# Kernel optimization log

Hardware: AMD Instinct MI355X
Metric: run time of the kernel (lower is better)

Reference implementation:

```python
import jax, jax.numpy as jnp
import numpy as np

B, N, L, D = 4096, 11, 12, 256
ZDIM = 32
LINE_DIM = 64
PAST_DIM = 6 * D - (2 * D + LINE_DIM)  # 960


def _pos_enc(length, d):
    # PositionalAgentEncoding.build_pos_enc
    pos = jnp.arange(length, dtype=jnp.float32)[:, None]
    div = jnp.exp(jnp.arange(0, d, 2, dtype=jnp.float32) * (-np.log(10000.0) / d))
    pe = jnp.zeros((length, d), dtype=jnp.float32)
    pe = pe.at[:, 0::2].set(jnp.sin(pos * div))
    pe = pe.at[:, 1::2].set(jnp.cos(pos * div))
    return pe


def setup_inputs() -> dict:
    key = jax.random.key(0)
    ks = jax.random.split(key, 16)
    s = 0.02
    return {
        "inputs": jax.random.normal(ks[0], (B * N, L, 4), jnp.float32),
        "past_feature": jax.random.normal(ks[1], (B * N, PAST_DIM), jnp.float32),
        "W_in": jax.random.normal(ks[2], (4, D), jnp.float32) * s,
        "b_in": jnp.zeros((D,), jnp.float32),
        "W_pos": jax.random.normal(ks[3], (2 * D, D), jnp.float32) * s,
        "b_pos": jnp.zeros((D,), jnp.float32),
        "W_fc2": jax.random.normal(ks[4], (L * D, D), jnp.float32) * s,
        "b_fc2": jnp.zeros((D,), jnp.float32),
        "W_fc3": jax.random.normal(ks[5], (D + N, D), jnp.float32) * s,
        "b_fc3": jnp.zeros((D,), jnp.float32),
        "W_msg": jax.random.normal(ks[6], (2 * D, D), jnp.float32) * s,
        "b_msg": jnp.zeros((D,), jnp.float32),
        "W_hyp": jax.random.normal(ks[7], (2 * D, D), jnp.float32) * s,
        "b_hyp": jnp.zeros((D,), jnp.float32),
        "W_line": jax.random.normal(ks[8], (D, LINE_DIM), jnp.float32) * s,
        "W_out": jax.random.normal(ks[9], (6 * D, 128), jnp.float32) * s,
        "b_out": jnp.zeros((128,), jnp.float32),
        "W_qz": jax.random.normal(ks[10], (128, 2 * ZDIM), jnp.float32) * s,
        "b_qz": jnp.zeros((2 * ZDIM,), jnp.float32),
        "batch_size": B,
        "agent_num": N,
    }


def reference(inputs, past_feature, W_in, b_in, W_pos, b_pos, W_fc2, b_fc2,
              W_fc3, b_fc3, W_msg, b_msg, W_hyp, b_hyp, W_line,
              W_out, b_out, W_qz, b_qz, batch_size, agent_num):
    BN, length, _ = inputs.shape
    d = W_in.shape[1]
    bsz, n = batch_size, agent_num
    # input_fc + positional encoding (concat=True, dropout=eval identity)
    tf = inputs @ W_in + b_in                                   # [BN, L, D]
    pe = jnp.broadcast_to(_pos_enc(length, d), (BN, length, d))
    tf = jnp.concatenate([tf, pe], axis=-1) @ W_pos + b_pos     # [BN, L, D]
    # input_fc2 over flattened time, then category concat + input_fc3
    ftraj = tf.reshape(bsz, n, length * d) @ W_fc2 + b_fc2      # [B, N, D]
    cat = jnp.broadcast_to(jnp.eye(n, dtype=ftraj.dtype), (bsz, n, n))
    ftraj = jnp.concatenate([ftraj, cat], axis=-1) @ W_fc3 + b_fc3
    # cosine correlation + per-scene adaptive threshold
    q = ftraj / jnp.linalg.norm(ftraj, axis=2, keepdims=True)
    corr = jnp.einsum('bnd,bmd->bnm', q, q)                     # [B, N, N]
    a = corr.min(axis=(1, 2))
    thr = jnp.where(a < 0.4, 0.4,
                    jnp.where((a > 0.4) & (a < 0.6), a + 0.1, a + 0.03))
    corr = jnp.where(corr < thr[:, None, None], 0.0, corr)
    # ordinary MS_HGNN surrogate: one dense message-passing round
    attn = jax.nn.softmax(jnp.einsum('bnd,bmd->bnm', ftraj, ftraj)
                          / jnp.sqrt(jnp.asarray(d, ftraj.dtype)), axis=-1)
    agg = jnp.einsum('bnm,bmd->bnd', attn, ftraj)
    ftraj_inter = jax.nn.relu(jnp.concatenate([ftraj, agg], -1) @ W_msg + b_msg)
    # hyper/clique surrogate: binarized thresholded corr as incidence, degree-normalized
    A = (corr > 0).astype(ftraj.dtype)
    A = A / jnp.maximum(A.sum(-1, keepdims=True), 1.0)
    hag = jnp.einsum('bnm,bmd->bnd', A, ftraj)
    hyp = jax.nn.relu(jnp.concatenate([ftraj, hag], -1) @ W_hyp + b_hyp)
    feat_bs = hyp @ W_line                                      # [B, N, 64]
    final = jnp.concatenate([ftraj, ftraj_inter, feat_bs], -1).reshape(bsz * n, -1)
    h = jnp.concatenate([past_feature, final], axis=-1)         # [BN, 6D]
    h = jax.nn.relu(h @ W_out + b_out)
    return h @ W_qz + b_qz                                      # [BN, 2*zdim]
```

## Files before the change

### kernel.cpp

```cpp
#include <hip/hip_runtime.h>
#include <hip/hip_bf16.h>

#define BB 4096
#define NNA 11
#define BN (BB*NNA)

#define OFF_WEFF   0
#define OFF_BIASL  1024
#define OFF_WBIG   4096
#define OFF_BIAS2  16384
#define OFF_WALL   16640
#define OFF_BIASN  28928
#define OFF_WG1F   31744
#define OFF_BIASG1 87040
#define OFF_WG2    99712
#define OFF_WQT    198656
#define OFF_P2T    202752
#define OFF_P3T    205824
#define OFF_MIX    296320
#define OFF_INTER  1287552

typedef short bh8 __attribute__((ext_vector_type(8)));
typedef float fx4 __attribute__((ext_vector_type(4)));

__device__ __forceinline__ short f2bs(float v) { __hip_bfloat16 h = __float2bfloat16(v); return *(short*)&h; }

typedef __attribute__((address_space(1))) const void __gptr_t;
typedef __attribute__((address_space(3))) void __lptr_t;
__device__ __forceinline__ void gload_lds16(const void* g, void* l) {
  __builtin_amdgcn_global_load_lds((__gptr_t*)g, (__lptr_t*)l, 16, 0, 0);
}


__global__ __launch_bounds__(256) void k_p1(const float* W_in, const float* b_in,
                                            const float* W_pos, const float* b_pos,
                                            float* ws) {
  __shared__ float A[16*512];
  __shared__ float red[4*16*64];
  int t = threadIdx.x, cb = blockIdx.x;
  int ks = t >> 6, c = t & 63, col = cb*64 + c;
  float coef = -logf(10000.f) / 256.f;
  for (int i = t; i < 16*512; i += 256) {
    int row = i >> 9, kk = i & 511;
    float v;
    if (row < 4) v = (kk < 256) ? W_in[row*256 + kk] : 0.f;
    else if (kk < 256) v = b_in[kk];
    else {
      int ii = (kk - 256) >> 1;
      float dv = expf(coef * (float)(2*ii));
      float ang = (float)(row - 4) * dv;
      v = (kk & 1) ? cosf(ang) : sinf(ang);
    }
    A[i] = v;
  }
  __syncthreads();
  float acc[16];
  #pragma unroll
  for (int r = 0; r < 16; ++r) acc[r] = 0.f;
  #pragma unroll 4
  for (int j = 0; j < 128; ++j) {
    int jj = ks*128 + j;
    float b = W_pos[(size_t)jj*256 + col];
    #pragma unroll
    for (int r = 0; r < 16; ++r) acc[r] += A[r*512 + jj] * b;
  }
  #pragma unroll
  for (int r = 0; r < 16; ++r) red[(ks*16 + r)*64 + c] = acc[r];
  __syncthreads();
  for (int i = t; i < 16*64; i += 256) {
    int row = i >> 6, cc = i & 63;
    float s = red[row*64+cc] + red[(16+row)*64+cc] + red[(32+row)*64+cc] + red[(48+row)*64+cc];
    int gcol = cb*64 + cc;
    if (row < 4) ws[OFF_WEFF + row*256 + gcol] = s;
    else         ws[OFF_BIASL + (row-4)*256 + gcol] = s + b_pos[gcol];
  }
}

__global__ __launch_bounds__(256) void k_p2(const float* W_fc2, float* ws) {
  __shared__ float A[5*256];
  __shared__ float red[4*5*64];
  int t = threadIdx.x, cb = blockIdx.x, l = blockIdx.y;
  int ks = t >> 6, c = t & 63, col = cb*64 + c;
  for (int i = t; i < 5*256; i += 256) {
    int row = i >> 8, kk = i & 255;
    A[i] = (row < 4) ? ws[OFF_WEFF + row*256 + kk] : ws[OFF_BIASL + l*256 + kk];
  }
  __syncthreads();
  float acc[5] = {0.f, 0.f, 0.f, 0.f, 0.f};
  #pragma unroll 4
  for (int j = 0; j < 64; ++j) {
    int jj = ks*64 + j;
    float b = W_fc2[(size_t)(l*256 + jj)*256 + col];
    #pragma unroll
    for (int r = 0; r < 5; ++r) acc[r] += A[r*256 + jj] * b;
  }
  #pragma unroll
  for (int r = 0; r < 5; ++r) red[(ks*5 + r)*64 + c] = acc[r];
  __syncthreads();
  for (int i = t; i < 5*64; i += 256) {
    int row = i / 64, cc = i % 64;
    float s = red[row*64+cc] + red[(5+row)*64+cc] + red[(10+row)*64+cc] + red[(15+row)*64+cc];
    int gcol = cb*64 + cc;
    if (row < 4) ws[OFF_WBIG + (l*4 + row)*256 + gcol] = s;
    else         ws[OFF_P2T + l*256 + gcol] = s;
  }
}

__global__ __launch_bounds__(256) void k_p3(const float* W_fc3, const float* b_fc2, float* ws) {
  __shared__ float A[7*256];
  __shared__ float red[4*7*64];
  int t = threadIdx.x, cb = blockIdx.x, rg = blockIdx.y;
  int ks = t >> 6, c = t & 63, col = cb*64 + c;
  for (int i = t; i < 7*256; i += 256) {
    int row = i >> 8, kk = i & 255, gr = rg*7 + row;
    float v;
    if (gr < 48) v = ws[OFF_WBIG + gr*256 + kk];
    else {
      v = b_fc2[kk];
      #pragma unroll
      for (int l = 0; l < 12; ++l) v += ws[OFF_P2T + l*256 + kk];
    }
    A[i] = v;
  }
  __syncthreads();
  float acc[7] = {0.f,0.f,0.f,0.f,0.f,0.f,0.f};
  #pragma unroll 4
  for (int j = 0; j < 64; ++j) {
    int jj = ks*64 + j;
    float b = W_fc3[(size_t)jj*256 + col];
    #pragma unroll
    for (int r = 0; r < 7; ++r) acc[r] += A[r*256 + jj] * b;
  }
  #pragma unroll
  for (int r = 0; r < 7; ++r) red[(ks*7 + r)*64 + c] = acc[r];
  __syncthreads();
  for (int i = t; i < 7*64; i += 256) {
    int row = i / 64, cc = i % 64, gr = rg*7 + row;
    float s = red[row*64+cc] + red[(7+row)*64+cc] + red[(14+row)*64+cc] + red[(21+row)*64+cc];
    int gcol = cb*64 + cc;
    if (gr < 48)       ws[OFF_WALL + gr*256 + gcol] = s;
    else if (gr == 48) ws[OFF_P3T + gcol] = s;
  }
}

__device__ __forceinline__ float wg1_elem(int j, int col, const float* W_msg,
                                          const float* W_hyp, const float* W_out) {
  if (col < 256)       return W_msg[j*256 + col];
  else if (col < 512)  return W_msg[(256+j)*256 + (col-256)];
  else if (col < 768)  return W_hyp[j*256 + (col-512)];
  else if (col < 1024) return W_hyp[(256+j)*256 + (col-768)];
  else                 return W_out[(960+j)*128 + (col-1024)];
}

__global__ __launch_bounds__(256) void k_p4(const float* W_msg, const float* b_msg,
                                            const float* W_hyp, const float* b_hyp,
                                            const float* W_out, const float* W_fc3,
                                            const float* b_fc3, float* ws) {
  __shared__ float A[8*256];
  __shared__ float red[4*8*64];
  int t = threadIdx.x, cb = blockIdx.x, rg = blockIdx.y;
  int ks = t >> 6, c = t & 63, col = cb*64 + c;
  for (int i = t; i < 8*256; i += 256) {
    int row = i >> 8, kk = i & 255, gr = rg*8 + row;
    float v;
    if (gr < 48)      v = ws[OFF_WALL + gr*256 + kk];
    else if (gr < 59) v = ws[OFF_P3T + kk] + b_fc3[kk] + W_fc3[(size_t)(256 + gr - 48)*256 + kk];
    else              v = 0.f;
    A[i] = v;
  }
  __syncthreads();
  float acc[8];
  #pragma unroll
  for (int r = 0; r < 8; ++r) acc[r] = 0.f;
  #pragma unroll 4
  for (int j = 0; j < 64; ++j) {
    int jj = ks*64 + j;
    float b = wg1_elem(jj, col, W_msg, W_hyp, W_out);
    #pragma unroll
    for (int r = 0; r < 8; ++r) acc[r] += A[r*256 + jj] * b;
  }
  #pragma unroll
  for (int r = 0; r < 8; ++r) red[(ks*8 + r)*64 + c] = acc[r];
  __syncthreads();
  for (int i = t; i < 8*64; i += 256) {
    int row = i >> 6, cc = i & 63, gr = rg*8 + row;
    float s = red[row*64+cc] + red[(8+row)*64+cc] + red[(16+row)*64+cc] + red[(24+row)*64+cc];
    int gcol = cb*64 + cc;
    if (gr < 48) {
      ws[OFF_WG1F + gr*1152 + gcol] = s;
    } else if (gr < 59) {
      if (gcol < 256) s += b_msg[gcol];
      else if (gcol >= 512 && gcol < 768) s += b_hyp[gcol-512];
      ws[OFF_BIASG1 + (gr-48)*1152 + gcol] = s;
    }
  }
}

__global__ __launch_bounds__(128) void k_p5(const float* W_line, const float* W_out,
                                            const float* W_qz, float* ws) {
  int t = threadIdx.x;
  if (blockIdx.x >= 1536) {
    int i = (blockIdx.x - 1536)*128 + t;
    int n = i >> 7, k = i & 127;
    short* WQs = (short*)(ws + OFF_WQT);
    WQs[n*128 + k] = f2bs(W_qz[k*64 + n]);
    return;
  }
  int c = t, r = blockIdx.x;
  float v;
  if (r < 960)       v = W_out[r*128 + c];
  else if (r < 1216) v = W_out[(r+256)*128 + c];
  else if (r < 1472) {
    int dd = r - 1216;
    float s = 0.f;
    for (int j = 0; j < 64; ++j)
      s += W_line[dd*64 + j] * W_out[(1472+j)*128 + c];
    v = s;
  } else if (r < 1520) {
    v = ws[OFF_WG1F + (r-1472)*1152 + 1024 + c];
  } else v = 0.f;
  short* WTs = (short*)(ws + OFF_WG2);
  WTs[(size_t)c*1536 + r] = f2bs(v);
}

__global__ __launch_bounds__(256) void k_front(const float* inputs, const float* W_fc3,
                                               const float* b_fc3, float* ws) {
  __shared__ float XT[48*44];
  __shared__ float F[44*260];
  __shared__ float C[4*121];
  int t = threadIdx.x;
  int R0 = blockIdx.x * 44;
  for (int i = t; i < 44*48; i += 256) {
    int r = i / 48, k = i - r*48;
    XT[k*44 + r] = inputs[(size_t)(R0+r)*48 + k];
  }
  __syncthreads();
  {
    int d = t;
    float acc[44];
    float base = ws[OFF_P3T + d] + b_fc3[d];
    #pragma unroll
    for (int r = 0; r < 44; ++r) acc[r] = base + W_fc3[(size_t)(256 + (r % 11))*256 + d];
    for (int k = 0; k < 48; ++k) {
      float w = ws[OFF_WALL + k*256 + d];
      #pragma unroll
      for (int j = 0; j < 11; ++j) {
        float4 xv = *(const float4*)&XT[k*44 + 4*j];
        acc[4*j+0] += xv.x*w; acc[4*j+1] += xv.y*w;
        acc[4*j+2] += xv.z*w; acc[4*j+3] += xv.w*w;
      }
    }
    #pragma unroll
    for (int r = 0; r < 44; ++r) F[r*260 + d] = acc[r];
  }
  __syncthreads();
  int w = t >> 6, lane = t & 63;
  {
    const float4* F4 = (const float4*)F;
    for (int p = lane; p < 66; p += 64) {
      int n = 0, pp = p;
      while (pp >= 11 - n) { pp -= 11 - n; ++n; }
      int m = n + pp;
      int ra = (w*11 + n) * 65, rb2 = (w*11 + m) * 65;
      float s = 0.f;
      #pragma unroll 4
      for (int j = 0; j < 64; ++j) {
        float4 a = F4[ra + j], b = F4[rb2 + j];
        s += a.x*b.x + a.y*b.y + a.z*b.z + a.w*b.w;
      }
      C[w*121 + n*11 + m] = s;
      C[w*121 + m*11 + n] = s;
    }
  }
  __syncthreads();
  {
    float* Cw = C + w*121;
    float rn[11];
    #pragma unroll
    for (int n = 0; n < 11; ++n) rn[n] = 1.f / sqrtf(Cw[n*11+n]);
    float a = 1e30f;
    for (int n = 0; n < 11; ++n)
      for (int m = 0; m < 11; ++m)
        a = fminf(a, Cw[n*11+m] * rn[n] * rn[m]);
    float thr = (a < 0.4f) ? 0.4f : (((a > 0.4f) && (a < 0.6f)) ? a + 0.1f : a + 0.03f);
    int scene = blockIdx.x*4 + w;
    float* mixb = ws + OFF_MIX + (size_t)scene*242;
    if (lane < 11) {
      int n = lane;
      float mx = -1e30f;
      #pragma unroll
      for (int m = 0; m < 11; ++m) mx = fmaxf(mx, Cw[n*11+m]);
      mx *= (1.f/16.f);
      float e[11], ssum = 0.f;
      #pragma unroll
      for (int m = 0; m < 11; ++m) { e[m] = expf(Cw[n*11+m]*(1.f/16.f) - mx); ssum += e[m]; }
      float inv = 1.f / ssum;
      #pragma unroll
      for (int m = 0; m < 11; ++m) mixb[n*11+m] = e[m]*inv;
      float keep[11], cnt = 0.f;
      #pragma unroll
      for (int m = 0; m < 11; ++m) {
        float q = Cw[n*11+m] * rn[n] * rn[m];
        keep[m] = (q >= thr) ? 1.f : 0.f; cnt += keep[m];
      }
      float sc = 1.f / fmaxf(cnt, 1.f);
      #pragma unroll
      for (int m = 0; m < 11; ++m) mixb[121 + n*11 + m] = keep[m]*sc;
    }
  }
}

__global__ __launch_bounds__(256) void k_mix(const float* inputs, float* ws,
                                             __hip_bfloat16* outI, __hip_bfloat16* outH) {
  __shared__ float XT[48*24];
  __shared__ float MW[2*121];
  int t = threadIdx.x;
  int s0 = blockIdx.x * 2;
  int R0 = s0 * 11;
  int gy = blockIdx.y;
  __hip_bfloat16* dst = gy ? outH : outI;
  for (int i = t; i < 22*48; i += 256) {
    int r = i / 48, k = i - r*48;
    XT[k*24 + r] = inputs[(size_t)(R0+r)*48 + k];
  }
  for (int i = t; i < 96; i += 256) { int k = i >> 1, r = 22 + (i & 1); XT[k*24+r] = 0.f; }
  for (int i = t; i < 242; i += 256) {
    int s = i / 121, j = i - s*121;
    MW[i] = ws[OFF_MIX + (size_t)(s0+s)*242 + gy*121 + j];
  }
  __syncthreads();
  int gc = gy*512 + t;
  float accT[24], accB[24];
  #pragma unroll
  for (int r = 0; r < 24; ++r) {
    if (r < 22) {
      accT[r] = ws[OFF_BIASG1 + (r % 11)*1152 + gc];
      accB[r] = ws[OFF_BIASG1 + (r % 11)*1152 + gc + 256];
    } else { accT[r] = 0.f; accB[r] = 0.f; }
  }
  for (int k = 0; k < 48; ++k) {
    float wt = ws[OFF_WG1F + k*1152 + gc];
    float wb = ws[OFF_WG1F + k*1152 + gc + 256];
    #pragma unroll
    for (int j = 0; j < 6; ++j) {
      float4 xv = *(const float4*)&XT[k*24 + 4*j];
      accT[4*j+0] += xv.x*wt; accT[4*j+1] += xv.y*wt; accT[4*j+2] += xv.z*wt; accT[4*j+3] += xv.w*wt;
      accB[4*j+0] += xv.x*wb; accB[4*j+1] += xv.y*wb; accB[4*j+2] += xv.z*wb; accB[4*j+3] += xv.w*wb;
    }
  }
  #pragma unroll
  for (int s = 0; s < 2; ++s)
    #pragma unroll
    for (int n = 0; n < 11; ++n) {
      float v = accT[s*11+n];
      #pragma unroll
      for (int m = 0; m < 11; ++m)
        v += MW[s*121 + n*11 + m] * accB[s*11+m];
      v = fmaxf(v, 0.f);
      dst[(size_t)(R0 + s*11 + n)*256 + t] = __float2bfloat16(v);
    }
}

#define A_BYTE(b) ((b)*8192)
#define B_BYTE(b) (16384 + (b)*16384)
#define HS_OFF 0
#define WQ_OFF 8704
__device__ __forceinline__ int swz(int row, int kshort) {
  return row*128 + ((kshort*2) ^ ((row & 7) << 4));
}
__global__ __launch_bounds__(256) void k_g2(const float* past, const float* inputs,
                                            const float* b_out, const float* b_qz,
                                            const __hip_bfloat16* interI, const __hip_bfloat16* hypI,
                                            float* ws, float* out) {
  __shared__ short LDS[24576];
  int t = threadIdx.x;
  int R0 = blockIdx.x * 64;
  int w = t >> 6, lane = t & 63, quad = lane >> 4, l16 = lane & 15;
  const short* WTs = (const short*)(ws + OFF_WG2);
  const short* WQs = (const short*)(ws + OFF_WQT);
  const short* intS = (const short*)interI;
  const short* hypS = (const short*)hypI;
  char* LB = (char*)LDS;

  int ar = t >> 2, akq = (t & 3) * 16;
  int brr = lane >> 3, bb0 = (lane & 7) * 16;

  fx4 acc[4][2];
  #pragma unroll
  for (int mt = 0; mt < 4; ++mt)
    #pragma unroll
    for (int reg = 0; reg < 4; ++reg) {
      int nidx = (R0 + mt*16 + quad*4 + reg) % 11;
      #pragma unroll
      for (int nt = 0; nt < 2; ++nt) {
        int col = w*32 + nt*16 + l16;
        acc[mt][nt][reg] = b_out[col] + ws[OFF_BIASG1 + nidx*1152 + 1024 + col];
      }
    }

  float4 pa[4];
  bh8 pah[2];

  auto prefA = [&](int cch) {
    if (cch < 15) {
      const float4* sp = (const float4*)(past + (size_t)(R0+ar)*960 + cch*64 + akq);
      pa[0]=sp[0]; pa[1]=sp[1]; pa[2]=sp[2]; pa[3]=sp[3];
    } else if (cch < 23) {
      const short* s = ((cch < 19) ? intS : hypS) + (size_t)(R0+ar)*256 + ((cch < 19)?(cch-15):(cch-19))*64 + akq;
      pah[0] = *(const bh8*)&s[0];
      pah[1] = *(const bh8*)&s[8];
    } else {
      if (akq < 48) {
        const float4* sp = (const float4*)(inputs + (size_t)(R0+ar)*48 + akq);
        pa[0]=sp[0]; pa[1]=sp[1]; pa[2]=sp[2]; pa[3]=sp[3];
      }
    }
  };
  auto writeA = [&](int cch, int abuf) {
    if (cch < 15 || cch == 23) {
      short tmp[16];
      if (cch == 23 && akq >= 48) {
        #pragma unroll
        for (int q = 0; q < 16; ++q) tmp[q] = 0;
      } else {
        #pragma unroll
        for (int q = 0; q < 4; ++q) {
          tmp[4*q+0]=f2bs(pa[q].x); tmp[4*q+1]=f2bs(pa[q].y);
          tmp[4*q+2]=f2bs(pa[q].z); tmp[4*q+3]=f2bs(pa[q].w);
        }
      }
      *(bh8*)(LB + A_BYTE(abuf) + swz(ar, akq))     = *(bh8*)&tmp[0];
      *(bh8*)(LB + A_BYTE(abuf) + swz(ar, akq + 8)) = *(bh8*)&tmp[8];
    } else {
      *(bh8*)(LB + A_BYTE(abuf) + swz(ar, akq))     = pah[0];
      *(bh8*)(LB + A_BYTE(abuf) + swz(ar, akq + 8)) = pah[1];
    }
  };
  auto stageB = [&](int cch, int bbuf) {
    #pragma unroll
    for (int c = 0; c < 4; ++c) {
      int r = (c*4 + w)*8 + brr;
      const char* g = (const char*)(WTs + (size_t)r*1536 + cch*64) + (bb0 ^ ((r & 7) << 4));
      gload_lds16(g, LB + B_BYTE(bbuf) + (c*4 + w)*1024);
    }
  };

  prefA(0);
  stageB(0, 0);
  writeA(0, 0);
  prefA(1);
  int buf = 0;
  for (int ch = 0; ch < 24; ++ch) {
    __syncthreads();
    if (ch + 1 < 24) {
      stageB(ch + 1, buf ^ 1);
      writeA(ch + 1, buf ^ 1);
      if (ch + 2 < 24) prefA(ch + 2);
    }
    #pragma unroll
    for (int ks = 0; ks < 2; ++ks) {
      int kk = ks*32 + quad*8;
      bh8 a[4], b[2];
      #pragma unroll
      for (int mt = 0; mt < 4; ++mt)
        a[mt] = *(const bh8*)(LB + A_BYTE(buf) + swz(mt*16 + l16, kk));
      #pragma unroll
      for (int nt = 0; nt < 2; ++nt) {
        int r = w*32 + nt*16 + l16;
        b[nt] = *(const bh8*)(LB + B_BYTE(buf) + swz(r, kk));
      }
      #pragma unroll
      for (int mt = 0; mt < 4; ++mt)
        #pragma unroll
        for (int nt = 0; nt < 2; ++nt)
          acc[mt][nt] = __builtin_amdgcn_mfma_f32_16x16x32_bf16(a[mt], b[nt], acc[mt][nt], 0, 0, 0);
    }
    buf ^= 1;
  }
  __syncthreads();
  #pragma unroll
  for (int mt = 0; mt < 4; ++mt)
    #pragma unroll
    for (int nt = 0; nt < 2; ++nt)
      #pragma unroll
      for (int reg = 0; reg < 4; ++reg)
        LDS[HS_OFF + (mt*16 + quad*4 + reg)*136 + w*32 + nt*16 + l16] = f2bs(fmaxf(acc[mt][nt][reg], 0.f));
  {
    int n = t >> 2, kh = (t & 3) * 32;
    const short* s = WQs + n*128 + kh;
    #pragma unroll
    for (int q = 0; q < 4; ++q)
      *(bh8*)&LDS[WQ_OFF + n*136 + kh + q*8] = *(const bh8*)&s[q*8];
  }
  __syncthreads();
  fx4 acc2[4];
  {
    float bq = b_qz[w*16 + l16];
    #pragma unroll
    for (int mt = 0; mt < 4; ++mt) { acc2[mt][0]=bq; acc2[mt][1]=bq; acc2[mt][2]=bq; acc2[mt][3]=bq; }
  }
  #pragma unroll
  for (int ks = 0; ks < 4; ++ks) {
    int kk = ks*32 + quad*8;
    bh8 bb = *(const bh8*)&LDS[WQ_OFF + (w*16 + l16)*136 + kk];
    #pragma unroll
    for (int mt = 0; mt < 4; ++mt) {
      bh8 aa = *(const bh8*)&LDS[HS_OFF + (mt*16 + l16)*136 + kk];
      acc2[mt] = __builtin_amdgcn_mfma_f32_16x16x32_bf16(aa, bb, acc2[mt], 0, 0, 0);
    }
  }
  #pragma unroll
  for (int mt = 0; mt < 4; ++mt)
    #pragma unroll
    for (int reg = 0; reg < 4; ++reg)
      out[(size_t)(R0 + mt*16 + quad*4 + reg)*64 + w*16 + l16] = acc2[mt][reg];
}

extern "C" void kernel_launch(void* const* d_in, const int* in_sizes, int n_in,
                              void* d_out, int out_size, void* d_ws, size_t ws_size,
                              hipStream_t stream) {
  const float* inputs = (const float*)d_in[0];
  const float* past   = (const float*)d_in[1];
  const float* W_in   = (const float*)d_in[2];
  const float* b_in   = (const float*)d_in[3];
  const float* W_pos  = (const float*)d_in[4];
  const float* b_pos  = (const float*)d_in[5];
  const float* W_fc2  = (const float*)d_in[6];
  const float* b_fc2  = (const float*)d_in[7];
  const float* W_fc3  = (const float*)d_in[8];
  const float* b_fc3  = (const float*)d_in[9];
  const float* W_msg  = (const float*)d_in[10];
  const float* b_msg  = (const float*)d_in[11];
  const float* W_hyp  = (const float*)d_in[12];
  const float* b_hyp  = (const float*)d_in[13];
  const float* W_line = (const float*)d_in[14];
  const float* W_out  = (const float*)d_in[15];
  const float* b_out  = (const float*)d_in[16];
  const float* W_qz   = (const float*)d_in[17];
  const float* b_qz   = (const float*)d_in[18];
  float* ws = (float*)d_ws;
  __hip_bfloat16* interI = (__hip_bfloat16*)(ws + OFF_INTER);
  __hip_bfloat16* hypI   = interI + (size_t)BN*256;
  float* outp   = (float*)d_out;

  hipLaunchKernelGGL(k_p1,  dim3(4),      dim3(256), 0, stream, W_in, b_in, W_pos, b_pos, ws);
  hipLaunchKernelGGL(k_p2,  dim3(4, 12),  dim3(256), 0, stream, W_fc2, ws);
  hipLaunchKernelGGL(k_p3,  dim3(4, 7),   dim3(256), 0, stream, W_fc3, b_fc2, ws);
  hipLaunchKernelGGL(k_p4,  dim3(18, 8),  dim3(256), 0, stream, W_msg, b_msg, W_hyp, b_hyp, W_out, W_fc3, b_fc3, ws);
  hipLaunchKernelGGL(k_p5,  dim3(1600),   dim3(128), 0, stream, W_line, W_out, W_qz, ws);
  hipLaunchKernelGGL(k_front, dim3(1024), dim3(256), 0, stream, inputs, W_fc3, b_fc3, ws);
  hipLaunchKernelGGL(k_mix, dim3(2048, 2), dim3(256), 0, stream, inputs, ws, interI, hypI);
  hipLaunchKernelGGL(k_g2,  dim3(704),    dim3(256), 0, stream, past, inputs, b_out, b_qz,
                     interI, hypI, ws, outp);
}
```

Baseline: 521.0 us.

## Load k_g2 GEMM operands directly from global into registers, dropping LDS staging

The k_g2 output GEMM no longer stages A and B tiles through double-buffered swizzled LDS. Each wave now loads its MFMA operand fragments straight from global memory (fp32 past/inputs converted to bf16 in registers, bf16 inter/hyp and weights read directly), with plain s_barriers between chunks to keep waves roughly in step. LDS shrinks and launch bounds request 4 blocks per CU to raise occupancy. The trade is that A rows are re-read by all four waves and the B weights by every block through L1/L2, with less coalesced access and no software prefetch to hide latency.

Result: slower. 574.6 us (+10.3%).

```diff
diff --git a/kernel.cpp b/kernel.cpp
--- a/kernel.cpp
+++ b/kernel.cpp
@@ -24,12 +24,6 @@
 typedef float fx4 __attribute__((ext_vector_type(4)));
 
 __device__ __forceinline__ short f2bs(float v) { __hip_bfloat16 h = __float2bfloat16(v); return *(short*)&h; }
-
-typedef __attribute__((address_space(1))) const void __gptr_t;
-typedef __attribute__((address_space(3))) void __lptr_t;
-__device__ __forceinline__ void gload_lds16(const void* g, void* l) {
-  __builtin_amdgcn_global_load_lds((__gptr_t*)g, (__lptr_t*)l, 16, 0, 0);
-}
 
 
 __global__ __launch_bounds__(256) void k_p1(const float* W_in, const float* b_in,
@@ -361,18 +355,13 @@
     }
 }
 
-#define A_BYTE(b) ((b)*8192)
-#define B_BYTE(b) (16384 + (b)*16384)
 #define HS_OFF 0
 #define WQ_OFF 8704
-__device__ __forceinline__ int swz(int row, int kshort) {
-  return row*128 + ((kshort*2) ^ ((row & 7) << 4));
-}
-__global__ __launch_bounds__(256) void k_g2(const float* past, const float* inputs,
+__global__ __launch_bounds__(256, 4) void k_g2(const float* past, const float* inputs,
                                             const float* b_out, const float* b_qz,
                                             const __hip_bfloat16* interI, const __hip_bfloat16* hypI,
                                             float* ws, float* out) {
-  __shared__ short LDS[24576];
+  __shared__ short LDS[17408];
   int t = threadIdx.x;
   int R0 = blockIdx.x * 64;
   int w = t >> 6, lane = t & 63, quad = lane >> 4, l16 = lane & 15;
@@ -380,10 +369,6 @@
   const short* WQs = (const short*)(ws + OFF_WQT);
   const short* intS = (const short*)interI;
   const short* hypS = (const short*)hypI;
-  char* LB = (char*)LDS;
-
-  int ar = t >> 2, akq = (t & 3) * 16;
-  int brr = lane >> 3, bb0 = (lane & 7) * 16;
 
   fx4 acc[4][2];
   #pragma unroll
@@ -398,86 +383,89 @@
       }
     }
 
-  float4 pa[4];
-  bh8 pah[2];
-
-  auto prefA = [&](int cch) {
-    if (cch < 15) {
-      const float4* sp = (const float4*)(past + (size_t)(R0+ar)*960 + cch*64 + akq);
-      pa[0]=sp[0]; pa[1]=sp[1]; pa[2]=sp[2]; pa[3]=sp[3];
-    } else if (cch < 23) {
-      const short* s = ((cch < 19) ? intS : hypS) + (size_t)(R0+ar)*256 + ((cch < 19)?(cch-15):(cch-19))*64 + akq;
-      pah[0] = *(const bh8*)&s[0];
-      pah[1] = *(const bh8*)&s[8];
-    } else {
-      if (akq < 48) {
-        const float4* sp = (const float4*)(inputs + (size_t)(R0+ar)*48 + akq);
-        pa[0]=sp[0]; pa[1]=sp[1]; pa[2]=sp[2]; pa[3]=sp[3];
-      }
-    }
-  };
-  auto writeA = [&](int cch, int abuf) {
-    if (cch < 15 || cch == 23) {
-      short tmp[16];
-      if (cch == 23 && akq >= 48) {
-        #pragma unroll
-        for (int q = 0; q < 16; ++q) tmp[q] = 0;
-      } else {
-        #pragma unroll
-        for (int q = 0; q < 4; ++q) {
-          tmp[4*q+0]=f2bs(pa[q].x); tmp[4*q+1]=f2bs(pa[q].y);
-          tmp[4*q+2]=f2bs(pa[q].z); tmp[4*q+3]=f2bs(pa[q].w);
+  const short* bp0 = WTs + (size_t)(w*32 + l16)*1536;
+  const short* bp1 = WTs + (size_t)(w*32 + 16 + l16)*1536;
+  const float* pr[4];
+  const short* ir[4];
+  const short* hr[4];
+  #pragma unroll
+  for (int mt = 0; mt < 4; ++mt) {
+    int row = R0 + mt*16 + l16;
+    pr[mt] = past + (size_t)row*960;
+    ir[mt] = intS + (size_t)row*256;
+    hr[mt] = hypS + (size_t)row*256;
+  }
+
+  for (int ch = 0; ch < 15; ++ch) {
+    #pragma unroll
+    for (int ks = 0; ks < 2; ++ks) {
+      int kq = ch*64 + ks*32 + quad*8;
+      bh8 b0 = *(const bh8*)(bp0 + kq);
+      bh8 b1 = *(const bh8*)(bp1 + kq);
+      #pragma unroll
+      for (int mt = 0; mt < 4; ++mt) {
+        const float4* ap = (const float4*)(pr[mt] + kq);
+        float4 v0 = ap[0], v1 = ap[1];
+        bh8 af;
+        af[0]=f2bs(v0.x); af[1]=f2bs(v0.y); af[2]=f2bs(v0.z); af[3]=f2bs(v0.w);
+        af[4]=f2bs(v1.x); af[5]=f2bs(v1.y); af[6]=f2bs(v1.z); af[7]=f2bs(v1.w);
+        acc[mt][0] = __builtin_amdgcn_mfma_f32_16x16x32_bf16(af, b0, acc[mt][0], 0, 0, 0);
+        acc[mt][1] = __builtin_amdgcn_mfma_f32_16x16x32_bf16(af, b1, acc[mt][1], 0, 0, 0);
+      }
+    }
+    __builtin_amdgcn_s_barrier();
+  }
+  for (int ch = 0; ch < 4; ++ch) {
+    #pragma unroll
+    for (int ks = 0; ks < 2; ++ks) {
+      int kq = ch*64 + ks*32 + quad*8;
+      bh8 b0 = *(const bh8*)(bp0 + 960 + kq);
+      bh8 b1 = *(const bh8*)(bp1 + 960 + kq);
+      #pragma unroll
+      for (int mt = 0; mt < 4; ++mt) {
+        bh8 af = *(const bh8*)(ir[mt] + kq);
+        acc[mt][0] = __builtin_amdgcn_mfma_f32_16x16x32_bf16(af, b0, acc[mt][0], 0, 0, 0);
+        acc[mt][1] = __builtin_amdgcn_mfma_f32_16x16x32_bf16(af, b1, acc[mt][1], 0, 0, 0);
+      }
+    }
+    __builtin_amdgcn_s_barrier();
+  }
+  for (int ch = 0; ch < 4; ++ch) {
+    #pragma unroll
+    for (int ks = 0; ks < 2; ++ks) {
+      int kq = ch*64 + ks*32 + quad*8;
+      bh8 b0 = *(const bh8*)(bp0 + 1216 + kq);
+      bh8 b1 = *(const bh8*)(bp1 + 1216 + kq);
+      #pragma unroll
+      for (int mt = 0; mt < 4; ++mt) {
+        bh8 af = *(const bh8*)(hr[mt] + kq);
+        acc[mt][0] = __builtin_amdgcn_mfma_f32_16x16x32_bf16(af, b0, acc[mt][0], 0, 0, 0);
+        acc[mt][1] = __builtin_amdgcn_mfma_f32_16x16x32_bf16(af, b1, acc[mt][1], 0, 0, 0);
+      }
+    }
+    __builtin_amdgcn_s_barrier();
+  }
+  {
+    #pragma unroll
+    for (int ks = 0; ks < 2; ++ks) {
+      int kq = ks*32 + quad*8;
+      bh8 b0 = *(const bh8*)(bp0 + 1472 + kq);
+      bh8 b1 = *(const bh8*)(bp1 + 1472 + kq);
+      #pragma unroll
+      for (int mt = 0; mt < 4; ++mt) {
+        bh8 af = {0,0,0,0,0,0,0,0};
+        if (kq < 48) {
+          const float4* ap = (const float4*)(inputs + (size_t)(R0 + mt*16 + l16)*48 + kq);
+          float4 v0 = ap[0], v1 = ap[1];
+          af[0]=f2bs(v0.x); af[1]=f2bs(v0.y); af[2]=f2bs(v0.z); af[3]=f2bs(v0.w);
+          af[4]=f2bs(v1.x); af[5]=f2bs(v1.y); af[6]=f2bs(v1.z); af[7]=f2bs(v1.w);
         }
-      }
-      *(bh8*)(LB + A_BYTE(abuf) + swz(ar, akq))     = *(bh8*)&tmp[0];
-      *(bh8*)(LB + A_BYTE(abuf) + swz(ar, akq + 8)) = *(bh8*)&tmp[8];
-    } else {
-      *(bh8*)(LB + A_BYTE(abuf) + swz(ar, akq))     = pah[0];
-      *(bh8*)(LB + A_BYTE(abuf) + swz(ar, akq + 8)) = pah[1];
-    }
-  };
-  auto stageB = [&](int cch, int bbuf) {
-    #pragma unroll
-    for (int c = 0; c < 4; ++c) {
-      int r = (c*4 + w)*8 + brr;
-      const char* g = (const char*)(WTs + (size_t)r*1536 + cch*64) + (bb0 ^ ((r & 7) << 4));
-      gload_lds16(g, LB + B_BYTE(bbuf) + (c*4 + w)*1024);
-    }
-  };
-
-  prefA(0);
-  stageB(0, 0);
-  writeA(0, 0);
-  prefA(1);
-  int buf = 0;
-  for (int ch = 0; ch < 24; ++ch) {
-    __syncthreads();
-    if (ch + 1 < 24) {
-      stageB(ch + 1, buf ^ 1);
-      writeA(ch + 1, buf ^ 1);
-      if (ch + 2 < 24) prefA(ch + 2);
-    }
-    #pragma unroll
-    for (int ks = 0; ks < 2; ++ks) {
-      int kk = ks*32 + quad*8;
-      bh8 a[4], b[2];
-      #pragma unroll
-      for (int mt = 0; mt < 4; ++mt)
-        a[mt] = *(const bh8*)(LB + A_BYTE(buf) + swz(mt*16 + l16, kk));
-      #pragma unroll
-      for (int nt = 0; nt < 2; ++nt) {
-        int r = w*32 + nt*16 + l16;
-        b[nt] = *(const bh8*)(LB + B_BYTE(buf) + swz(r, kk));
-      }
-      #pragma unroll
-      for (int mt = 0; mt < 4; ++mt)
-        #pragma unroll
-        for (int nt = 0; nt < 2; ++nt)
-          acc[mt][nt] = __builtin_amdgcn_mfma_f32_16x16x32_bf16(a[mt], b[nt], acc[mt][nt], 0, 0, 0);
-    }
-    buf ^= 1;
-  }
-  __syncthreads();
+        acc[mt][0] = __builtin_amdgcn_mfma_f32_16x16x32_bf16(af, b0, acc[mt][0], 0, 0, 0);
+        acc[mt][1] = __builtin_amdgcn_mfma_f32_16x16x32_bf16(af, b1, acc[mt][1], 0, 0, 0);
+      }
+    }
+  }
+
   #pragma unroll
   for (int mt = 0; mt < 4; ++mt)
     #pragma unroll
```
